# Kernel tuning notes

Hardware: AMD Instinct MI355X
Metric: run time of the kernel (lower is better)

The kernel has to match this reference:

```python
import jax, jax.numpy as jnp
import numpy as np

N, D_IN, D_HID, D_OUT, E = 100000, 128, 256, 64, 1600000


def setup_inputs() -> dict:
    key = jax.random.key(0)
    ks = jax.random.split(key, 6)
    x = jax.random.normal(ks[0], (N, D_IN), dtype=jnp.float32)
    edge_index = jax.random.randint(ks[1], (2, E), 0, N, dtype=jnp.int64)
    # Linear params (PyTorch convention: y = x @ W.T + b)
    W1 = jax.random.normal(ks[2], (D_HID, D_IN), dtype=jnp.float32) / np.sqrt(D_IN)
    b1 = jax.random.normal(ks[3], (D_HID,), dtype=jnp.float32) * 0.01
    W2 = jax.random.normal(ks[4], (D_OUT, D_HID), dtype=jnp.float32) / np.sqrt(D_HID)
    b2 = jax.random.normal(ks[5], (D_OUT,), dtype=jnp.float32) * 0.01
    return {"x": x, "edge_index": edge_index, "W1": W1, "b1": b1, "W2": W2, "b2": b2}


def _scatter_mean(vals, dst, num_nodes):
    # sum neighbor features per destination node, divide by in-degree (0-degree -> 0)
    s = jax.ops.segment_sum(vals, dst, num_segments=num_nodes)
    cnt = jax.ops.segment_sum(jnp.ones((dst.shape[0],), vals.dtype), dst, num_segments=num_nodes)
    return s / jnp.maximum(cnt, 1.0)[:, None]


def _sage_layer(x, src, dst, W, b):
    neighbors = x[src]                      # [E, d] gather
    agg = _scatter_mean(neighbors, dst, x.shape[0])  # [N, d]
    return agg @ W.T + b


def reference(x, edge_index, W1, b1, W2, b2):
    src, dst = edge_index[0], edge_index[1]
    h = _sage_layer(x, src, dst, W1, b1)
    h = jax.nn.relu(h)
    # dropout is identity at inference (training=False)
    y = _sage_layer(h, src, dst, W2, b2)
    return jax.nn.log_softmax(y, axis=1)
```

## Files before the change

kernel.cpp:

```cpp
#include <hip/hip_runtime.h>


typedef __attribute__((ext_vector_type(8))) short bf16x8;
typedef __attribute__((ext_vector_type(4))) float f32x4;
typedef __attribute__((ext_vector_type(2))) float f32x2;

#define BSHIFT 10
#define BMASK  1023
#define SRCMASK 0x1FFFF
#define TBIN   4096

#if __has_builtin(__builtin_amdgcn_cvt_pk_f32_fp8) && __has_builtin(__builtin_amdgcn_cvt_pk_fp8_f32)
#define HAVE_FP8_CVT 1
#else
#define HAVE_FP8_CVT 0
#endif

__device__ inline ushort f2bf(float f) {
  union { float f; unsigned u; } c; c.f = f;
  unsigned r = (c.u + 0x7fffu + ((c.u >> 16) & 1u)) >> 16;
  return (ushort)r;
}

#if HAVE_FP8_CVT
template <bool HI>
__device__ inline f32x2 fp8x2f(unsigned w) {
  return __builtin_amdgcn_cvt_pk_f32_fp8((int)w, HI);
}
template <bool HI>
__device__ inline unsigned fp8pack2(unsigned old, float a, float b) {
  return (unsigned)__builtin_amdgcn_cvt_pk_fp8_f32(a, b, (int)old, HI);
}
#else
__device__ inline float fp8tof_1(unsigned b) {
  unsigned e = (b >> 3) & 15u, m = b & 7u;
  float v;
  if (e == 0) v = (float)m * 0x1p-9f;
  else { union { unsigned u; float f; } c; c.u = ((e + 120u) << 23) | (m << 20); v = c.f; }
  return (b & 0x80u) ? -v : v;
}
template <bool HI>
__device__ inline f32x2 fp8x2f(unsigned w) {
  unsigned sh = HI ? 16 : 0;
  f32x2 r;
  r.x = fp8tof_1((w >> sh) & 0xFFu);
  r.y = fp8tof_1((w >> (sh + 8)) & 0xFFu);
  return r;
}
__device__ inline unsigned f2fp8_1(float f) {
  float af = fabsf(f);
  unsigned s = (f < 0.f) ? 0x80u : 0u;
  if (!(af < 448.f)) return s | 0x7Eu;
  if (af < 0x1p-6f) {
    int m = (int)rintf(af * 512.0f);
    if (m >= 8) return s | 0x08u;
    return s | (unsigned)m;
  }
  int e;
  frexpf(af, &e);
  int E = e - 1;
  int q = (int)rintf(ldexpf(af, 3 - E));
  if (q >= 16) { q = 8; E += 1; if (E > 8) return s | 0x7Eu; }
  return s | ((unsigned)(E + 7) << 3) | ((unsigned)q & 7u);
}
template <bool HI>
__device__ inline unsigned fp8pack2(unsigned old, float a, float b) {
  unsigned pair = f2fp8_1(a) | (f2fp8_1(b) << 8);
  return HI ? ((old & 0x0000FFFFu) | (pair << 16)) : ((old & 0xFFFF0000u) | pair);
}
#endif

__global__ void __launch_bounds__(64) k_detect(const int* __restrict__ ei, int* __restrict__ flag,
                                               unsigned long long* __restrict__ xpad,
                                               unsigned long long* __restrict__ gpad) {
  int t = threadIdx.x;
  int v = ei[2 * t + 1];
  unsigned long long m = __ballot(v != 0);
  if (t == 0) *flag = (m == 0ull) ? 1 : 0;
  if (t < 16) xpad[t] = 0ull;
  if (t < 8)  gpad[t] = 0ull;
}

__global__ void __launch_bounds__(256) k_prep_x(const float4* __restrict__ x4, uint2* __restrict__ xq8, int total8) {
  int i = blockIdx.x * 256 + threadIdx.x;
  if (i >= total8) return;
  float4 v0 = x4[2 * i], v1 = x4[2 * i + 1];
  unsigned w0 = fp8pack2<false>(0u, v0.x, v0.y);
  w0 = fp8pack2<true>(w0, v0.z, v0.w);
  unsigned w1 = fp8pack2<false>(0u, v1.x, v1.y);
  w1 = fp8pack2<true>(w1, v1.z, v1.w);
  xq8[i] = make_uint2(w0, w1);
}

__global__ void __launch_bounds__(256) k_prep_w(const float* __restrict__ W1, const float* __restrict__ W2,
                                                ushort* __restrict__ W1f, ushort* __restrict__ W2f) {
  int idx = blockIdx.x * 256 + threadIdx.x;
  if (idx < 32768) {
    int jt = idx >> 11, rem = idx & 2047;
    int kt = rem >> 9, rem2 = rem & 511;
    int l = rem2 >> 3, e = rem2 & 7;
    int k = kt * 32 + (l >> 4) * 8 + e;
    int j = jt * 16 + (l & 15);
    W1f[idx] = f2bf(W1[j * 128 + k]);
  } else {
    int i2 = idx - 32768;
    if (i2 < 16384) {
      int ot = i2 >> 12, rem = i2 & 4095;
      int kt = rem >> 9;
      int l = (rem >> 3) & 63, e = rem & 7;
      int k = kt * 32 + (l >> 4) * 8 + e;
      int o = ot * 16 + (l & 15);
      W2f[i2] = f2bf(W2[o * 256 + k]);
    }
  }
}

__global__ void __launch_bounds__(256) k_bhist(const int* __restrict__ ei, const int* __restrict__ flag,
                                               int* __restrict__ bcnt, int E, int NB) {
  __shared__ int h[128];
  int t = threadIdx.x;
  if (t < 128) h[t] = 0;
  __syncthreads();
  bool f64 = (*flag != 0);
  int stride = gridDim.x * 256;
  for (int e = blockIdx.x * 256 + t; e < E; e += stride) {
    int d;
    if (f64) d = (int)((const long long*)ei)[(size_t)E + e];
    else     d = ei[(size_t)E + e];
    atomicAdd(&h[d >> BSHIFT], 1);
  }
  __syncthreads();
  if (t < NB && h[t]) atomicAdd(&bcnt[t], h[t]);
}

__global__ void __launch_bounds__(128) k_bscan(const int* __restrict__ bcnt, int* __restrict__ bbase,
                                               int* __restrict__ bcur, int* __restrict__ row_ptr,
                                               int NB, int N, int E) {
  __shared__ int s[128];
  int t = threadIdx.x;
  int v = (t < NB) ? bcnt[t] : 0;
  s[t] = v;
  __syncthreads();
  for (int o = 1; o < 128; o <<= 1) {
    int u = (t >= o) ? s[t - o] : 0;
    __syncthreads();
    s[t] += u;
    __syncthreads();
  }
  if (t < NB) {
    int base = s[t] - v;
    bbase[t] = base;
    bcur[t] = base;
  }
  if (t == 0) {
    bbase[NB] = E;
    row_ptr[N] = E;
  }
}

__global__ void __launch_bounds__(256) k_bin(const int* __restrict__ ei, const int* __restrict__ flag,
                                             int* __restrict__ bcur, int* __restrict__ gpair, int E, int NB) {
  __shared__ int hist[128], base[128], segb[128], cur[128], scanb[128];
  __shared__ int ent[TBIN];
  __shared__ int gdx[TBIN];
  int t = threadIdx.x;
  int e0 = blockIdx.x * TBIN;
  int cnt = E - e0; if (cnt > TBIN) cnt = TBIN;
  if (t < 128) hist[t] = 0;
  __syncthreads();
  bool f64 = (*flag != 0);
  int ment[16], mbk[16];
#pragma unroll
  for (int i = 0; i < 16; ++i) {
    int idx = t + i * 256;
    mbk[i] = -1;
    if (idx < cnt) {
      int e = e0 + idx;
      int s, d;
      if (f64) {
        const long long* p = (const long long*)ei;
        s = (int)p[e];
        d = (int)p[(size_t)E + e];
      } else {
        s = ei[e];
        d = ei[(size_t)E + e];
      }
      int b = d >> BSHIFT;
      mbk[i] = b;
      ment[i] = ((d & BMASK) << 17) | s;
      atomicAdd(&hist[b], 1);
    }
  }
  __syncthreads();
  if (t < 128) scanb[t] = hist[t];
  __syncthreads();
  for (int o = 1; o < 128; o <<= 1) {
    int u = 0;
    if (t < 128 && t >= o) u = scanb[t - o];
    __syncthreads();
    if (t < 128) scanb[t] += u;
    __syncthreads();
  }
  if (t < 128) {
    int b0 = scanb[t] - hist[t];
    base[t] = b0;
    cur[t] = b0;
    segb[t] = (t < NB && hist[t] > 0) ? atomicAdd(&bcur[t], hist[t]) : 0;
  }
  __syncthreads();
#pragma unroll
  for (int i = 0; i < 16; ++i) {
    int b = mbk[i];
    if (b >= 0) {
      int pos = atomicAdd(&cur[b], 1);
      ent[pos] = ment[i];
      gdx[pos] = segb[b] + (pos - base[b]);
    }
  }
  __syncthreads();
  for (int i = t; i < cnt; i += 256) gpair[gdx[i]] = ent[i];
}

__global__ void __launch_bounds__(1024) k_bcsr(const int* __restrict__ gpair, const int* __restrict__ bbase,
                                               int* __restrict__ row_ptr, float* __restrict__ inv_deg,
                                               int* __restrict__ csr, int N) {
  __shared__ int hist[1024], pre[1024], cur[1024];
  int b = blockIdx.x, t = threadIdx.x;
  int start = bbase[b], end = bbase[b + 1];
  hist[t] = 0;
  __syncthreads();
  for (int i = start + t; i < end; i += 1024) {
    int e = gpair[i];
    atomicAdd(&hist[e >> 17], 1);
  }
  __syncthreads();
  pre[t] = hist[t];
  __syncthreads();
  for (int o = 1; o < 1024; o <<= 1) {
    int u = (t >= o) ? pre[t - o] : 0;
    __syncthreads();
    pre[t] += u;
    __syncthreads();
  }
  int gbase = start + pre[t] - hist[t];
  int n = (b << BSHIFT) + t;
  if (n < N) {
    row_ptr[n] = gbase;
    inv_deg[n] = 1.0f / (float)(hist[t] > 0 ? hist[t] : 1);
  }
  cur[t] = gbase;
  __syncthreads();
  for (int i = start + t; i < end; i += 1024) {
    int e = gpair[i];
    int pos = atomicAdd(&cur[e >> 17], 1);
    csr[pos] = e & SRCMASK;
  }
}

__global__ void __launch_bounds__(256) k_agg1(const unsigned char* __restrict__ xq, const int* __restrict__ csr,
                                              const int* __restrict__ row_ptr, const float* __restrict__ inv_deg,
                                              ushort* __restrict__ agg1b, int N) {
  const int lane = threadIdx.x & 63;
  const int g = lane >> 4;
  const int g16 = lane & 48;
  const int p = lane & 15;
  const int h = (lane >> 3) & 1;
  const int c = lane & 7;
  const unsigned coff = (unsigned)c * 16u;
  const int shbase = g16 + h;

  const int NQ = (N + 3) >> 2;
  const int tw = gridDim.x * 4;
  int quad = (blockIdx.x * 256 + threadIdx.x) >> 6;
  if (quad >= NQ) return;
  int rp = quad * 4 + (lane < 4 ? lane : 4);
  if (rp > N) rp = N;
  int rv = row_ptr[rp];

  for (;;) {
    const int qn = quad + tw;
    int rvn = 0;
    if (qn < NQ) {
      int rpn = qn * 4 + (lane < 4 ? lane : 4);
      if (rpn > N) rpn = N;
      rvn = row_ptr[rpn];
    }
    const int n = quad * 4 + g;
    const int s = __shfl(rv, g);
    const int cnt = __shfl(rv, g + 1) - s;
    int maxc = cnt;
    maxc = max(maxc, __shfl_xor(maxc, 16));
    maxc = max(maxc, __shfl_xor(maxc, 32));

    f32x2 a[8];
#pragma unroll
    for (int i = 0; i < 8; ++i) a[i] = (f32x2)(0.f);

    for (int base = 0; base < maxc; base += 16) {
      int li = base + p;
      int ci = (li < cnt) ? csr[s + li] : N;
#pragma unroll
      for (int u = 0; u < 8; ++u) {
        int idx = __shfl(ci, shbase + 2 * u);
        unsigned off = ((unsigned)idx << 7) + coff;
        const uint4 wv = *(const uint4*)(xq + off);
        a[0] += fp8x2f<false>(wv.x); a[1] += fp8x2f<true>(wv.x);
        a[2] += fp8x2f<false>(wv.y); a[3] += fp8x2f<true>(wv.y);
        a[4] += fp8x2f<false>(wv.z); a[5] += fp8x2f<true>(wv.z);
        a[6] += fp8x2f<false>(wv.w); a[7] += fp8x2f<true>(wv.w);
      }
    }
#pragma unroll
    for (int i = 0; i < 8; ++i) {
      a[i].x += __shfl_xor(a[i].x, 8);
      a[i].y += __shfl_xor(a[i].y, 8);
    }
    if (n < N) {
      const float inv = inv_deg[n];
      bf16x8 o;
#pragma unroll
      for (int k = 0; k < 4; ++k) {
        f32x2 v0 = a[k], v1 = a[k + 4];
        float vx = h ? v1.x : v0.x;
        float vy = h ? v1.y : v0.y;
        o[2 * k]     = (short)f2bf(vx * inv);
        o[2 * k + 1] = (short)f2bf(vy * inv);
      }
      *(bf16x8*)(agg1b + (size_t)n * 128 + c * 16 + h * 8) = o;
    }
    if (qn >= NQ) break;
    quad = qn; rv = rvn;
  }
}

__global__ void __launch_bounds__(256) k_mlp(const ushort* __restrict__ agg1b, const bf16x8* __restrict__ w1f,
                                             const float* __restrict__ b1, const bf16x8* __restrict__ w2f,
                                             unsigned char* __restrict__ gq, int N) {
  __shared__ __align__(16) ushort sm[16896];
  ushort* aT = sm;
  ushort* hT = sm;
  const int t = threadIdx.x;
  const int n0 = blockIdx.x * 64;

#pragma unroll
  for (int i = 0; i < 4; ++i) {
    int idx = i * 256 + t;
    int row = idx >> 4, c8 = idx & 15;
    int rr = n0 + row; if (rr >= N) rr = N - 1;
    bf16x8 v = *(const bf16x8*)(agg1b + (size_t)rr * 128 + c8 * 8);
    *(bf16x8*)(aT + row * 136 + c8 * 8) = v;
  }
  __syncthreads();

  const int w = t >> 6, l = t & 63;
  const int lm = l & 15, lq = l >> 4;

  f32x4 acc[4][4];
#pragma unroll
  for (int mt = 0; mt < 4; ++mt)
#pragma unroll
    for (int nt = 0; nt < 4; ++nt) acc[mt][nt] = (f32x4)(0.f);

#pragma unroll
  for (int kt = 0; kt < 4; ++kt) {
    bf16x8 b[4], a[4];
#pragma unroll
    for (int nt = 0; nt < 4; ++nt)
      b[nt] = w1f[((w * 4 + nt) * 4 + kt) * 64 + l];
#pragma unroll
    for (int mt = 0; mt < 4; ++mt)
      a[mt] = *(const bf16x8*)(aT + (mt * 16 + lm) * 136 + kt * 32 + lq * 8);
#pragma unroll
    for (int mt = 0; mt < 4; ++mt)
#pragma unroll
      for (int nt = 0; nt < 4; ++nt)
        acc[mt][nt] = __builtin_amdgcn_mfma_f32_16x16x32_bf16(a[mt], b[nt], acc[mt][nt], 0, 0, 0);
  }
  __syncthreads();

#pragma unroll
  for (int nt = 0; nt < 4; ++nt) {
    int col = w * 64 + nt * 16 + lm;
    float bb = b1[col];
#pragma unroll
    for (int mt = 0; mt < 4; ++mt)
#pragma unroll
      for (int r = 0; r < 4; ++r) {
        int row = mt * 16 + lq * 4 + r;
        float hv = acc[mt][nt][r] + bb;
        hT[row * 264 + col] = f2bf(fmaxf(hv, 0.f));
      }
  }
  __syncthreads();

  f32x4 acc2[4];
#pragma unroll
  for (int ot = 0; ot < 4; ++ot) acc2[ot] = (f32x4)(0.f);
#pragma unroll
  for (int kt = 0; kt < 8; ++kt) {
    bf16x8 a2 = *(const bf16x8*)(hT + (w * 16 + lm) * 264 + kt * 32 + lq * 8);
#pragma unroll
    for (int ot = 0; ot < 4; ++ot) {
      bf16x8 bf = w2f[(ot * 8 + kt) * 64 + l];
      acc2[ot] = __builtin_amdgcn_mfma_f32_16x16x32_bf16(a2, bf, acc2[ot], 0, 0, 0);
    }
  }
#pragma unroll
  for (int ot = 0; ot < 4; ++ot)
#pragma unroll
    for (int r = 0; r < 4; ++r) {
      int row = n0 + w * 16 + lq * 4 + r;
      if (row < N) {
        unsigned pw = fp8pack2<false>(0u, acc2[ot][r], acc2[ot][r]);
        gq[(size_t)row * 64 + ot * 16 + lm] = (unsigned char)(pw & 0xFFu);
      }
    }
}

__global__ void __launch_bounds__(256) k_agg2(const unsigned char* __restrict__ gq, const int* __restrict__ csr,
                                              const int* __restrict__ row_ptr, const float* __restrict__ inv_deg,
                                              const float* __restrict__ b2, float* __restrict__ out, int N) {
  const int lane = threadIdx.x & 63;
  const int g = lane >> 4;
  const int g16 = lane & 48;
  const int p = lane & 15;
  const int q2 = (lane >> 2) & 3;
  const int c = lane & 3;
  const unsigned coff = (unsigned)c * 16u;
  const int shbase = g16 + q2;

  const int NQ = (N + 3) >> 2;
  const int tw = gridDim.x * 4;
  int quad = (blockIdx.x * 256 + threadIdx.x) >> 6;
  if (quad >= NQ) return;
  int rp = quad * 4 + (lane < 4 ? lane : 4);
  if (rp > N) rp = N;
  int rv = row_ptr[rp];

  float4 bv0 = *(const float4*)(b2 + c * 16);
  float4 bv1 = *(const float4*)(b2 + c * 16 + 4);
  float4 bv2 = *(const float4*)(b2 + c * 16 + 8);
  float4 bv3 = *(const float4*)(b2 + c * 16 + 12);

  for (;;) {
    const int qn = quad + tw;
    int rvn = 0;
    if (qn < NQ) {
      int rpn = qn * 4 + (lane < 4 ? lane : 4);
      if (rpn > N) rpn = N;
      rvn = row_ptr[rpn];
    }
    const int n = quad * 4 + g;
    const int s = __shfl(rv, g);
    const int cnt = __shfl(rv, g + 1) - s;
    int maxc = cnt;
    maxc = max(maxc, __shfl_xor(maxc, 16));
    maxc = max(maxc, __shfl_xor(maxc, 32));

    f32x2 a[8];
#pragma unroll
    for (int i = 0; i < 8; ++i) a[i] = (f32x2)(0.f);

    for (int base = 0; base < maxc; base += 16) {
      int li = base + p;
      int ci = (li < cnt) ? csr[s + li] : N;
#pragma unroll
      for (int u = 0; u < 4; ++u) {
        int idx = __shfl(ci, shbase + 4 * u);
        unsigned off = ((unsigned)idx << 6) + coff;
        const uint4 wv = *(const uint4*)(gq + off);
        a[0] += fp8x2f<false>(wv.x); a[1] += fp8x2f<true>(wv.x);
        a[2] += fp8x2f<false>(wv.y); a[3] += fp8x2f<true>(wv.y);
        a[4] += fp8x2f<false>(wv.z); a[5] += fp8x2f<true>(wv.z);
        a[6] += fp8x2f<false>(wv.w); a[7] += fp8x2f<true>(wv.w);
      }
    }
#pragma unroll
    for (int i = 0; i < 8; ++i) {
      a[i].x += __shfl_xor(a[i].x, 4); a[i].y += __shfl_xor(a[i].y, 4);
      a[i].x += __shfl_xor(a[i].x, 8); a[i].y += __shfl_xor(a[i].y, 8);
    }
    const float inv = inv_deg[n < N ? n : 0];
    float v[16];
    v[0]  = a[0].x * inv + bv0.x;  v[1]  = a[0].y * inv + bv0.y;
    v[2]  = a[1].x * inv + bv0.z;  v[3]  = a[1].y * inv + bv0.w;
    v[4]  = a[2].x * inv + bv1.x;  v[5]  = a[2].y * inv + bv1.y;
    v[6]  = a[3].x * inv + bv1.z;  v[7]  = a[3].y * inv + bv1.w;
    v[8]  = a[4].x * inv + bv2.x;  v[9]  = a[4].y * inv + bv2.y;
    v[10] = a[5].x * inv + bv2.z;  v[11] = a[5].y * inv + bv2.w;
    v[12] = a[6].x * inv + bv3.x;  v[13] = a[6].y * inv + bv3.y;
    v[14] = a[7].x * inv + bv3.z;  v[15] = a[7].y * inv + bv3.w;
    float mx = v[0];
#pragma unroll
    for (int j = 1; j < 16; ++j) mx = fmaxf(mx, v[j]);
    mx = fmaxf(mx, __shfl_xor(mx, 1));
    mx = fmaxf(mx, __shfl_xor(mx, 2));
    float se = 0.f;
#pragma unroll
    for (int j = 0; j < 16; ++j) se += expf(v[j] - mx);
    se += __shfl_xor(se, 1);
    se += __shfl_xor(se, 2);
    float lse = mx + logf(se);
    if (n < N && q2 == 0) {
      float* po = out + (size_t)n * 64 + c * 16;
      float4 o0, o1, o2, o3;
      o0.x = v[0] - lse;  o0.y = v[1] - lse;  o0.z = v[2] - lse;  o0.w = v[3] - lse;
      o1.x = v[4] - lse;  o1.y = v[5] - lse;  o1.z = v[6] - lse;  o1.w = v[7] - lse;
      o2.x = v[8] - lse;  o2.y = v[9] - lse;  o2.z = v[10] - lse; o2.w = v[11] - lse;
      o3.x = v[12] - lse; o3.y = v[13] - lse; o3.z = v[14] - lse; o3.w = v[15] - lse;
      *(float4*)(po)      = o0;
      *(float4*)(po + 4)  = o1;
      *(float4*)(po + 8)  = o2;
      *(float4*)(po + 12) = o3;
    }
    if (qn >= NQ) break;
    quad = qn; rv = rvn;
  }
}

extern "C" void kernel_launch(void* const* d_in, const int* in_sizes, int n_in,
                              void* d_out, int out_size, void* d_ws, size_t ws_size,
                              hipStream_t stream) {
  const float* x  = (const float*)d_in[0];
  const int*   ei = (const int*)d_in[1];
  const float* W1 = (const float*)d_in[2];
  const float* b1 = (const float*)d_in[3];
  const float* W2 = (const float*)d_in[4];
  const float* b2 = (const float*)d_in[5];
  float* out = (float*)d_out;
  const int N = in_sizes[0] / 128;
  const int E = in_sizes[1] / 2;
  const int NB = (N + BMASK) >> BSHIFT;

  char* base = (char*)d_ws;
  size_t off = 0;
  auto alloc = [&](size_t bytes) -> char* {
    char* p = base + off;
    off += (bytes + 255) & ~(size_t)255;
    return p;
  };
  int*    flag    = (int*)alloc(4);
  int*    bcnt    = (int*)alloc((size_t)NB * 4);
  int*    bbase   = (int*)alloc((size_t)(NB + 1) * 4);
  int*    bcur    = (int*)alloc((size_t)NB * 4);
  int*    gpair   = (int*)alloc((size_t)E * 4);
  int*    row_ptr = (int*)alloc((size_t)(N + 1) * 4);
  float*  inv_deg = (float*)alloc((size_t)N * 4);
  int*    csr     = (int*)alloc((size_t)E * 4);
  unsigned char* xq = (unsigned char*)alloc((size_t)(N + 1) * 128);
  ushort* W1f     = (ushort*)alloc((size_t)32768 * 2);
  ushort* W2f     = (ushort*)alloc((size_t)16384 * 2);
  ushort* agg1b   = (ushort*)alloc((size_t)N * 128 * 2);
  unsigned char* gq = (unsigned char*)alloc((size_t)(N + 1) * 64);
  (void)ws_size; (void)n_in; (void)out_size;

  hipMemsetAsync(bcnt, 0, (size_t)NB * 4, stream);
  k_detect<<<1, 64, 0, stream>>>(ei, flag,
                                 (unsigned long long*)(xq + (size_t)N * 128),
                                 (unsigned long long*)(gq + (size_t)N * 64));
  k_prep_x<<<(N * 16 + 255) / 256, 256, 0, stream>>>((const float4*)x, (uint2*)xq, N * 16);
  k_prep_w<<<192, 256, 0, stream>>>(W1, W2, W1f, W2f);
  k_bhist<<<512, 256, 0, stream>>>(ei, flag, bcnt, E, NB);
  k_bscan<<<1, 128, 0, stream>>>(bcnt, bbase, bcur, row_ptr, NB, N, E);
  k_bin<<<(E + TBIN - 1) / TBIN, 256, 0, stream>>>(ei, flag, bcur, gpair, E, NB);
  k_bcsr<<<NB, 1024, 0, stream>>>(gpair, bbase, row_ptr, inv_deg, csr, N);
  k_agg1<<<2048, 256, 0, stream>>>(xq, csr, row_ptr, inv_deg, agg1b, N);
  k_mlp<<<(N + 63) / 64, 256, 0, stream>>>(agg1b, (const bf16x8*)W1f, b1, (const bf16x8*)W2f, gq, N);
  k_agg2<<<2048, 256, 0, stream>>>(gq, csr, row_ptr, inv_deg, b2, out, N);
}
```

Measured before the change: 272.3 us.

## Replace grid-stride loops in aggregation kernels with one-quad-per-wave grids and prefetch

Both aggregation kernels drop the persistent grid-stride loop and launch one wavefront per group of four nodes. The inner neighbour loop is restructured so all gathers in a chunk are issued before any fp8 conversion, and the next chunk's CSR indices are prefetched. k_agg2 also processes 32 neighbours per iteration. The aim is more memory-level parallelism and better latency hiding, at the cost of more registers and a much larger grid.

```diff
diff --git a/kernel.cpp b/kernel.cpp
--- a/kernel.cpp
+++ b/kernel.cpp
@@ -269,67 +269,59 @@
   const unsigned coff = (unsigned)c * 16u;
   const int shbase = g16 + h;
 
-  const int NQ = (N + 3) >> 2;
-  const int tw = gridDim.x * 4;
-  int quad = (blockIdx.x * 256 + threadIdx.x) >> 6;
-  if (quad >= NQ) return;
-  int rp = quad * 4 + (lane < 4 ? lane : 4);
+  const int quad = blockIdx.x * 4 + (threadIdx.x >> 6);
+  const int n0 = quad * 4;
+  if (n0 >= N) return;
+  int rp = n0 + (lane < 4 ? lane : 4);
   if (rp > N) rp = N;
-  int rv = row_ptr[rp];
-
-  for (;;) {
-    const int qn = quad + tw;
-    int rvn = 0;
-    if (qn < NQ) {
-      int rpn = qn * 4 + (lane < 4 ? lane : 4);
-      if (rpn > N) rpn = N;
-      rvn = row_ptr[rpn];
-    }
-    const int n = quad * 4 + g;
-    const int s = __shfl(rv, g);
-    const int cnt = __shfl(rv, g + 1) - s;
-    int maxc = cnt;
-    maxc = max(maxc, __shfl_xor(maxc, 16));
-    maxc = max(maxc, __shfl_xor(maxc, 32));
-
-    f32x2 a[8];
-#pragma unroll
-    for (int i = 0; i < 8; ++i) a[i] = (f32x2)(0.f);
-
-    for (int base = 0; base < maxc; base += 16) {
-      int li = base + p;
-      int ci = (li < cnt) ? csr[s + li] : N;
-#pragma unroll
-      for (int u = 0; u < 8; ++u) {
-        int idx = __shfl(ci, shbase + 2 * u);
-        unsigned off = ((unsigned)idx << 7) + coff;
-        const uint4 wv = *(const uint4*)(xq + off);
-        a[0] += fp8x2f<false>(wv.x); a[1] += fp8x2f<true>(wv.x);
-        a[2] += fp8x2f<false>(wv.y); a[3] += fp8x2f<true>(wv.y);
-        a[4] += fp8x2f<false>(wv.z); a[5] += fp8x2f<true>(wv.z);
-        a[6] += fp8x2f<false>(wv.w); a[7] += fp8x2f<true>(wv.w);
-      }
-    }
-#pragma unroll
-    for (int i = 0; i < 8; ++i) {
-      a[i].x += __shfl_xor(a[i].x, 8);
-      a[i].y += __shfl_xor(a[i].y, 8);
-    }
-    if (n < N) {
-      const float inv = inv_deg[n];
-      bf16x8 o;
-#pragma unroll
-      for (int k = 0; k < 4; ++k) {
-        f32x2 v0 = a[k], v1 = a[k + 4];
-        float vx = h ? v1.x : v0.x;
-        float vy = h ? v1.y : v0.y;
-        o[2 * k]     = (short)f2bf(vx * inv);
-        o[2 * k + 1] = (short)f2bf(vy * inv);
-      }
-      *(bf16x8*)(agg1b + (size_t)n * 128 + c * 16 + h * 8) = o;
-    }
-    if (qn >= NQ) break;
-    quad = qn; rv = rvn;
+  const int rv = row_ptr[rp];
+  const int n = n0 + g;
+  const int s = __shfl(rv, g);
+  const int cnt = __shfl(rv, g + 1) - s;
+  int maxc = cnt;
+  maxc = max(maxc, __shfl_xor(maxc, 16));
+  maxc = max(maxc, __shfl_xor(maxc, 32));
+
+  f32x2 a[8];
+#pragma unroll
+  for (int i = 0; i < 8; ++i) a[i] = (f32x2)(0.f);
+
+  int ci = (p < cnt) ? csr[s + p] : N;
+  for (int base = 0; base < maxc; base += 16) {
+    uint4 wv[8];
+#pragma unroll
+    for (int u = 0; u < 8; ++u) {
+      int idx = __shfl(ci, shbase + 2 * u);
+      wv[u] = *(const uint4*)(xq + (((unsigned)idx << 7) + coff));
+    }
+    int li = base + 16 + p;
+    int cin = (li < cnt) ? csr[s + li] : N;
+#pragma unroll
+    for (int u = 0; u < 8; ++u) {
+      a[0] += fp8x2f<false>(wv[u].x); a[1] += fp8x2f<true>(wv[u].x);
+      a[2] += fp8x2f<false>(wv[u].y); a[3] += fp8x2f<true>(wv[u].y);
+      a[4] += fp8x2f<false>(wv[u].z); a[5] += fp8x2f<true>(wv[u].z);
+      a[6] += fp8x2f<false>(wv[u].w); a[7] += fp8x2f<true>(wv[u].w);
+    }
+    ci = cin;
+  }
+#pragma unroll
+  for (int i = 0; i < 8; ++i) {
+    a[i].x += __shfl_xor(a[i].x, 8);
+    a[i].y += __shfl_xor(a[i].y, 8);
+  }
+  if (n < N) {
+    const float inv = inv_deg[n];
+    bf16x8 o;
+#pragma unroll
+    for (int k = 0; k < 4; ++k) {
+      f32x2 v0 = a[k], v1 = a[k + 4];
+      float vx = h ? v1.x : v0.x;
+      float vy = h ? v1.y : v0.y;
+      o[2 * k]     = (short)f2bf(vx * inv);
+      o[2 * k + 1] = (short)f2bf(vy * inv);
+    }
+    *(bf16x8*)(agg1b + (size_t)n * 128 + c * 16 + h * 8) = o;
   }
 }
 
@@ -429,92 +421,91 @@
   const unsigned coff = (unsigned)c * 16u;
   const int shbase = g16 + q2;
 
-  const int NQ = (N + 3) >> 2;
-  const int tw = gridDim.x * 4;
-  int quad = (blockIdx.x * 256 + threadIdx.x) >> 6;
-  if (quad >= NQ) return;
-  int rp = quad * 4 + (lane < 4 ? lane : 4);
+  const int quad = blockIdx.x * 4 + (threadIdx.x >> 6);
+  const int n0 = quad * 4;
+  if (n0 >= N) return;
+  int rp = n0 + (lane < 4 ? lane : 4);
   if (rp > N) rp = N;
-  int rv = row_ptr[rp];
-
+  const int rv = row_ptr[rp];
+  const int n = n0 + g;
+  const int s = __shfl(rv, g);
+  const int cnt = __shfl(rv, g + 1) - s;
+  int maxc = cnt;
+  maxc = max(maxc, __shfl_xor(maxc, 16));
+  maxc = max(maxc, __shfl_xor(maxc, 32));
+
+  f32x2 a[8];
+#pragma unroll
+  for (int i = 0; i < 8; ++i) a[i] = (f32x2)(0.f);
+
+  int ci0 = (p < cnt) ? csr[s + p] : N;
+  int li1 = 16 + p;
+  int ci1 = (li1 < cnt) ? csr[s + li1] : N;
+  for (int base = 0; base < maxc; base += 32) {
+    uint4 wv[8];
+#pragma unroll
+    for (int u = 0; u < 4; ++u) {
+      int idx = __shfl(ci0, shbase + 4 * u);
+      wv[u] = *(const uint4*)(gq + (((unsigned)idx << 6) + coff));
+    }
+#pragma unroll
+    for (int u = 0; u < 4; ++u) {
+      int idx = __shfl(ci1, shbase + 4 * u);
+      wv[4 + u] = *(const uint4*)(gq + (((unsigned)idx << 6) + coff));
+    }
+    int li2 = base + 32 + p, li3 = base + 48 + p;
+    int cin0 = (li2 < cnt) ? csr[s + li2] : N;
+    int cin1 = (li3 < cnt) ? csr[s + li3] : N;
+#pragma unroll
+    for (int u = 0; u < 8; ++u) {
+      a[0] += fp8x2f<false>(wv[u].x); a[1] += fp8x2f<true>(wv[u].x);
+      a[2] += fp8x2f<false>(wv[u].y); a[3] += fp8x2f<true>(wv[u].y);
+      a[4] += fp8x2f<false>(wv[u].z); a[5] += fp8x2f<true>(wv[u].z);
+      a[6] += fp8x2f<false>(wv[u].w); a[7] += fp8x2f<true>(wv[u].w);
+    }
+    ci0 = cin0; ci1 = cin1;
+  }
+#pragma unroll
+  for (int i = 0; i < 8; ++i) {
+    a[i].x += __shfl_xor(a[i].x, 4); a[i].y += __shfl_xor(a[i].y, 4);
+    a[i].x += __shfl_xor(a[i].x, 8); a[i].y += __shfl_xor(a[i].y, 8);
+  }
+  const float inv = inv_deg[n < N ? n : 0];
   float4 bv0 = *(const float4*)(b2 + c * 16);
   float4 bv1 = *(const float4*)(b2 + c * 16 + 4);
   float4 bv2 = *(const float4*)(b2 + c * 16 + 8);
   float4 bv3 = *(const float4*)(b2 + c * 16 + 12);
-
-  for (;;) {
-    const int qn = quad + tw;
-    int rvn = 0;
-    if (qn < NQ) {
-      int rpn = qn * 4 + (lane < 4 ? lane : 4);
-      if (rpn > N) rpn = N;
-      rvn = row_ptr[rpn];
-    }
-    const int n = quad * 4 + g;
-    const int s = __shfl(rv, g);
-    const int cnt = __shfl(rv, g + 1) - s;
-    int maxc = cnt;
-    maxc = max(maxc, __shfl_xor(maxc, 16));
-    maxc = max(maxc, __shfl_xor(maxc, 32));
-
-    f32x2 a[8];
-#pragma unroll
-    for (int i = 0; i < 8; ++i) a[i] = (f32x2)(0.f);
-
-    for (int base = 0; base < maxc; base += 16) {
-      int li = base + p;
-      int ci = (li < cnt) ? csr[s + li] : N;
-#pragma unroll
-      for (int u = 0; u < 4; ++u) {
-        int idx = __shfl(ci, shbase + 4 * u);
-        unsigned off = ((unsigned)idx << 6) + coff;
-        const uint4 wv = *(const uint4*)(gq + off);
-        a[0] += fp8x2f<false>(wv.x); a[1] += fp8x2f<true>(wv.x);
-        a[2] += fp8x2f<false>(wv.y); a[3] += fp8x2f<true>(wv.y);
-        a[4] += fp8x2f<false>(wv.z); a[5] += fp8x2f<true>(wv.z);
-        a[6] += fp8x2f<false>(wv.w); a[7] += fp8x2f<true>(wv.w);
-      }
-    }
-#pragma unroll
-    for (int i = 0; i < 8; ++i) {
-      a[i].x += __shfl_xor(a[i].x, 4); a[i].y += __shfl_xor(a[i].y, 4);
-      a[i].x += __shfl_xor(a[i].x, 8); a[i].y += __shfl_xor(a[i].y, 8);
-    }
-    const float inv = inv_deg[n < N ? n : 0];
-    float v[16];
-    v[0]  = a[0].x * inv + bv0.x;  v[1]  = a[0].y * inv + bv0.y;
-    v[2]  = a[1].x * inv + bv0.z;  v[3]  = a[1].y * inv + bv0.w;
-    v[4]  = a[2].x * inv + bv1.x;  v[5]  = a[2].y * inv + bv1.y;
-    v[6]  = a[3].x * inv + bv1.z;  v[7]  = a[3].y * inv + bv1.w;
-    v[8]  = a[4].x * inv + bv2.x;  v[9]  = a[4].y * inv + bv2.y;
-    v[10] = a[5].x * inv + bv2.z;  v[11] = a[5].y * inv + bv2.w;
-    v[12] = a[6].x * inv + bv3.x;  v[13] = a[6].y * inv + bv3.y;
-    v[14] = a[7].x * inv + bv3.z;  v[15] = a[7].y * inv + bv3.w;
-    float mx = v[0];
-#pragma unroll
-    for (int j = 1; j < 16; ++j) mx = fmaxf(mx, v[j]);
-    mx = fmaxf(mx, __shfl_xor(mx, 1));
-    mx = fmaxf(mx, __shfl_xor(mx, 2));
-    float se = 0.f;
-#pragma unroll
-    for (int j = 0; j < 16; ++j) se += expf(v[j] - mx);
-    se += __shfl_xor(se, 1);
-    se += __shfl_xor(se, 2);
-    float lse = mx + logf(se);
-    if (n < N && q2 == 0) {
-      float* po = out + (size_t)n * 64 + c * 16;
-      float4 o0, o1, o2, o3;
-      o0.x = v[0] - lse;  o0.y = v[1] - lse;  o0.z = v[2] - lse;  o0.w = v[3] - lse;
-      o1.x = v[4] - lse;  o1.y = v[5] - lse;  o1.z = v[6] - lse;  o1.w = v[7] - lse;
-      o2.x = v[8] - lse;  o2.y = v[9] - lse;  o2.z = v[10] - lse; o2.w = v[11] - lse;
-      o3.x = v[12] - lse; o3.y = v[13] - lse; o3.z = v[14] - lse; o3.w = v[15] - lse;
-      *(float4*)(po)      = o0;
-      *(float4*)(po + 4)  = o1;
-      *(float4*)(po + 8)  = o2;
-      *(float4*)(po + 12) = o3;
-    }
-    if (qn >= NQ) break;
-    quad = qn; rv = rvn;
+  float v[16];
+  v[0]  = a[0].x * inv + bv0.x;  v[1]  = a[0].y * inv + bv0.y;
+  v[2]  = a[1].x * inv + bv0.z;  v[3]  = a[1].y * inv + bv0.w;
+  v[4]  = a[2].x * inv + bv1.x;  v[5]  = a[2].y * inv + bv1.y;
+  v[6]  = a[3].x * inv + bv1.z;  v[7]  = a[3].y * inv + bv1.w;
+  v[8]  = a[4].x * inv + bv2.x;  v[9]  = a[4].y * inv + bv2.y;
+  v[10] = a[5].x * inv + bv2.z;  v[11] = a[5].y * inv + bv2.w;
+  v[12] = a[6].x * inv + bv3.x;  v[13] = a[6].y * inv + bv3.y;
+  v[14] = a[7].x * inv + bv3.z;  v[15] = a[7].y * inv + bv3.w;
+  float mx = v[0];
+#pragma unroll
+  for (int j = 1; j < 16; ++j) mx = fmaxf(mx, v[j]);
+  mx = fmaxf(mx, __shfl_xor(mx, 1));
+  mx = fmaxf(mx, __shfl_xor(mx, 2));
+  float se = 0.f;
+#pragma unroll
+  for (int j = 0; j < 16; ++j) se += expf(v[j] - mx);
+  se += __shfl_xor(se, 1);
+  se += __shfl_xor(se, 2);
+  float lse = mx + logf(se);
+  if (n < N && q2 == 0) {
+    float* po = out + (size_t)n * 64 + c * 16;
+    float4 o0, o1, o2, o3;
+    o0.x = v[0] - lse;  o0.y = v[1] - lse;  o0.z = v[2] - lse;  o0.w = v[3] - lse;
+    o1.x = v[4] - lse;  o1.y = v[5] - lse;  o1.z = v[6] - lse;  o1.w = v[7] - lse;
+    o2.x = v[8] - lse;  o2.y = v[9] - lse;  o2.z = v[10] - lse; o2.w = v[11] - lse;
+    o3.x = v[12] - lse; o3.y = v[13] - lse; o3.z = v[14] - lse; o3.w = v[15] - lse;
+    *(float4*)(po)      = o0;
+    *(float4*)(po + 4)  = o1;
+    *(float4*)(po + 8)  = o2;
+    *(float4*)(po + 12) = o3;
   }
 }
 
@@ -564,7 +555,7 @@
   k_bscan<<<1, 128, 0, stream>>>(bcnt, bbase, bcur, row_ptr, NB, N, E);
   k_bin<<<(E + TBIN - 1) / TBIN, 256, 0, stream>>>(ei, flag, bcur, gpair, E, NB);
   k_bcsr<<<NB, 1024, 0, stream>>>(gpair, bbase, row_ptr, inv_deg, csr, N);
-  k_agg1<<<2048, 256, 0, stream>>>(xq, csr, row_ptr, inv_deg, agg1b, N);
+  k_agg1<<<(N + 15) / 16, 256, 0, stream>>>(xq, csr, row_ptr, inv_deg, agg1b, N);
   k_mlp<<<(N + 63) / 64, 256, 0, stream>>>(agg1b, (const bf16x8*)W1f, b1, (const bf16x8*)W2f, gq, N);
-  k_agg2<<<2048, 256, 0, stream>>>(gq, csr, row_ptr, inv_deg, b2, out, N);
-}
+  k_agg2<<<(N + 15) / 16, 256, 0, stream>>>(gq, csr, row_ptr, inv_deg, b2, out, N);
+}
```

Result: faster. 248.0 us (-8.9%).
